# Kernel tuning notes

Hardware: AMD Instinct MI355X
Metric: run time of the kernel (lower is better)

The kernel has to match this reference:

```python
import jax, jax.numpy as jnp
import numpy as np

B, L, D = 4, 1024, 1024
H, DK, DV = 16, 64, 64
TEMP = float(np.power(DK, 0.5))
LN_EPS = 1e-5


def setup_inputs() -> dict:
    key = jax.random.key(0)
    ks = jax.random.split(key, 11)
    s_qk = np.sqrt(2.0 / (D + DK))
    s_v = np.sqrt(2.0 / (D + DV))
    inp = {
        'q_in': jax.random.normal(ks[0], (B, L, D), jnp.float32),
        'k_in': jax.random.normal(ks[1], (B, L, D), jnp.float32),
        'v_in': jax.random.normal(ks[2], (B, L, D), jnp.float32),
        'Wq':  jax.random.normal(ks[3], (D, H * DK), jnp.float32) * s_qk,
        'Wq2': jax.random.normal(ks[4], (D, H * DK), jnp.float32) * s_qk,
        'Wk':  jax.random.normal(ks[5], (D, H * DK), jnp.float32) * s_qk,
        'Wv':  jax.random.normal(ks[6], (D, H * DV), jnp.float32) * s_v,
        'Wo':  jax.random.normal(ks[7], (H * DV, D), jnp.float32) * np.sqrt(2.0 / (H * DV + D)),
        'ln_g': jnp.ones((D,), jnp.float32),
        'ln_b': jnp.zeros((D,), jnp.float32),
        'Er':  jax.random.normal(ks[8], (H, L, DK), jnp.float32),
        # causal mask: True above the diagonal (positions to be masked with -inf)
        'mask': jnp.triu(jnp.ones((L, L), jnp.bool_), k=1)[None].repeat(B, axis=0),
    }
    return inp


def _skew(rel):
    # rel: [H, B, Lq, Lr] with Lr == Lq. Music-Transformer skew:
    # pad one zero column on the left, reshape, drop first row.
    h, b, lq, lr = rel.shape
    rel = jnp.pad(rel, ((0, 0), (0, 0), (0, 0), (1, 0)))        # [H,B,Lq,Lr+1]
    rel = rel.reshape(h, b, lr + 1, lq)                          # [H,B,Lr+1,Lq]
    return rel[:, :, 1:, :].reshape(h, b, lq, lr)                # [H,B,Lq,Lr]


def reference(q_in, k_in, v_in, Wq, Wq2, Wk, Wv, Wo, ln_g, ln_b, Er, mask):
    residual = q_in
    # projections -> [H, B, L, d]
    def proj(x, W, d):
        return x.reshape(B * L, D).dot(W).reshape(B, L, H, d).transpose(2, 0, 1, 3)
    q = proj(q_in, Wq, DK)
    q2 = proj(q_in, Wq2, DK)
    k = proj(k_in, Wk, DK)
    v = proj(v_in, Wv, DV)

    attn = jnp.einsum('hbqd,hbkd->hbqk', q, k) / TEMP            # [H,B,Lq,Lk]
    rel = _skew(jnp.einsum('hbqd,hrd->hbqr', q2, Er)) / TEMP     # [H,B,Lq,Lk]

    m = mask[None]                                               # [1,B,Lq,Lk]
    neg = jnp.float32(-jnp.inf)
    attn = jnp.where(m, neg, attn)
    rel = jnp.where(m, neg, rel)
    p = jax.nn.softmax(attn + rel, axis=-1)                      # [H,B,Lq,Lk]

    out = jnp.einsum('hbqk,hbkd->hbqd', p, v)                    # [H,B,Lq,DV]
    out = out.transpose(1, 2, 0, 3).reshape(B, L, H * DV)
    out = out.dot(Wo)                                            # dropout is identity (eval)

    x = out + residual
    mu = x.mean(-1, keepdims=True)
    var = x.var(-1, keepdims=True)
    y = (x - mu) * jax.lax.rsqrt(var + LN_EPS) * ln_g + ln_b
    return y, p
```

## Files before the change

### kernel.cpp

```cpp
#include <hip/hip_runtime.h>

typedef __bf16 bf16;
typedef __bf16 v8bf __attribute__((ext_vector_type(8)));
typedef float v4f __attribute__((ext_vector_type(4)));
typedef unsigned int v4u __attribute__((ext_vector_type(4)));

#define B_ 4
#define L_ 1024
#define D_ 1024
#define NEG (-3.0e38f)
#define MFMA16(a, b, c) __builtin_amdgcn_mfma_f32_16x16x32_bf16(a, b, c, 0, 0, 0)

#define SWZ(base, r, cb) ((char*)(base) + ((r) * 128) + ((cb) ^ (((r) & 7) << 4)))

typedef const __attribute__((address_space(1))) void* gas_t;
typedef __attribute__((address_space(3))) void* las_t;
__device__ __forceinline__ void gl_lds16(const bf16* g, bf16* l)
{
    __builtin_amdgcn_global_load_lds((gas_t)g, (las_t)l, 16, 0, 0);
}

__global__ __launch_bounds__(256) void wconv_kernel(
    const float* __restrict__ w0, const float* __restrict__ w1,
    const float* __restrict__ w2, const float* __restrict__ w3,
    const float* __restrict__ w4, const float* __restrict__ er,
    const float* __restrict__ qin, const float* __restrict__ kin,
    const float* __restrict__ vin,
    bf16* __restrict__ wt, bf16* __restrict__ erb,
    bf16* __restrict__ qbf, bf16* __restrict__ kbf, bf16* __restrict__ vbf)
{
    int z = blockIdx.z;
    int tx = threadIdx.x, ty = threadIdx.y;
    if (z < 5) {
        const float* src = z == 0 ? w0 : z == 1 ? w1 : z == 2 ? w2 : z == 3 ? w3 : w4;
        bf16* dst = wt + (size_t)z * 1024 * 1024;
        __shared__ float t[32][33];
        int bx = blockIdx.x * 32, by = blockIdx.y * 32;
#pragma unroll
        for (int i = 0; i < 4; i++)
            t[ty + i * 8][tx] = src[(size_t)(by + ty + i * 8) * 1024 + bx + tx];
        __syncthreads();
#pragma unroll
        for (int i = 0; i < 4; i++)
            dst[(size_t)(bx + ty + i * 8) * 1024 + by + tx] = (bf16)t[tx][ty + i * 8];
    } else if (z == 5) {
        int base = (blockIdx.y * 32 + blockIdx.x) * 256 + ty * 32 + tx;
#pragma unroll
        for (int i = 0; i < 4; i++) {
            int idx = base + i * 262144;
            erb[idx] = (bf16)er[idx];
        }
    } else {
        const float* src = z == 6 ? qin : z == 7 ? kin : vin;
        bf16* dst = z == 6 ? qbf : z == 7 ? kbf : vbf;
        int id = (blockIdx.y * 32 + blockIdx.x) * 256 + ty * 32 + tx;
#pragma unroll
        for (int i = 0; i < 4; i++) {
            int j = id * 4 + i * 1048576;
            float4 v = *(const float4*)(src + j);
            union { bf16 h[4]; uint2 u; } t;
            t.h[0] = (bf16)v.x; t.h[1] = (bf16)v.y;
            t.h[2] = (bf16)v.z; t.h[3] = (bf16)v.w;
            *(uint2*)(dst + j) = t.u;
        }
    }
}

__global__ __launch_bounds__(256) void gemm64(
    const bf16* __restrict__ Ab, const bf16* __restrict__ Bt,
    float* __restrict__ Cf, bf16* __restrict__ Cb, bf16* __restrict__ Cb2,
    int K, int mode)
{
    __shared__ __align__(16) bf16 As[2][64 * 32];
    __shared__ __align__(16) bf16 Bs[2][128 * 32];
    int tid = threadIdx.x, lane = tid & 63, w = tid >> 6;
    int tn = blockIdx.x * 128, tm = blockIdx.y * 64;
    int wn = w * 32;
    int m15 = lane & 15, rq = lane >> 4, kq = rq * 8;

    v4f acc[4][2];
#pragma unroll
    for (int m = 0; m < 4; ++m)
#pragma unroll
        for (int n = 0; n < 2; ++n)
#pragma unroll
            for (int i = 0; i < 4; ++i) acc[m][n][i] = 0.f;

    int sr = lane >> 2, sc8 = (lane & 3) * 8;
    const bf16* ga  = Ab + (size_t)(tm + w * 16 + sr) * K + sc8;
    const bf16* gb0 = Bt + (size_t)(tn + w * 32 + sr) * K + sc8;
    const bf16* gb1 = gb0 + (size_t)16 * K;

#define GSTAGE(buf, k0s) { \
    gl_lds16(ga  + (k0s), As[buf] + w * 16 * 32); \
    gl_lds16(gb0 + (k0s), Bs[buf] + w * 32 * 32); \
    gl_lds16(gb1 + (k0s), Bs[buf] + (w * 32 + 16) * 32); }

    int cur = 0;
    GSTAGE(0, 0);
    __syncthreads();
    for (int k0 = 0; k0 < K; k0 += 32) {
        if (k0 + 32 < K) GSTAGE(cur ^ 1, k0 + 32);
        v8bf a[4], bb[2];
#pragma unroll
        for (int m = 0; m < 4; ++m)
            a[m] = *(const v8bf*)&As[cur][(m * 16 + m15) * 32 + kq];
#pragma unroll
        for (int n = 0; n < 2; ++n)
            bb[n] = *(const v8bf*)&Bs[cur][(wn + n * 16 + m15) * 32 + kq];
#pragma unroll
        for (int m = 0; m < 4; ++m)
#pragma unroll
            for (int n = 0; n < 2; ++n)
                acc[m][n] = MFMA16(a[m], bb[n], acc[m][n]);
        __syncthreads();
        cur ^= 1;
    }
#undef GSTAGE

#pragma unroll
    for (int m = 0; m < 4; ++m)
#pragma unroll
        for (int n = 0; n < 2; ++n) {
            int col = tn + wn + n * 16 + m15;
            if (mode == 2) {
                union { bf16 h[4]; uint2 u; } pk;
#pragma unroll
                for (int i = 0; i < 4; ++i) pk.h[i] = (bf16)acc[m][n][i];
                int row0 = tm + m * 16 + rq * 4;
                int bb2 = row0 >> 10, l = row0 & 1023, hh = col >> 6, dv = col & 63;
                *(uint2*)&Cb[(((size_t)(bb2 * 16 + hh) * 64 + dv) << 10) + l] = pk.u;
            } else {
#pragma unroll
                for (int i = 0; i < 4; ++i) {
                    int row = tm + m * 16 + rq * 4 + i;
                    float v = acc[m][n][i];
                    if (mode == 1) Cf[(size_t)row * 1024 + col] = v;
                    else {
                        bf16* dst = col < 1024 ? Cb : Cb2;
                        dst[(size_t)row * 1024 + (col & 1023)] = (bf16)v;
                    }
                }
            }
        }
}

__global__ __launch_bounds__(256, 2) void attn_mfma(
    const bf16* __restrict__ qb, const bf16* __restrict__ q2b,
    const bf16* __restrict__ kb, const bf16* __restrict__ vt,
    const bf16* __restrict__ erb, float* __restrict__ p_out,
    bf16* __restrict__ ab)
{
    int lin = blockIdx.x;
    int bh  = (lin & 7) | ((lin >> 6) << 3);
    int pp  = (lin >> 3) & 7;
    int h = bh >> 2, b = bh & 3;
    int tid = threadIdx.x, lane = tid & 63, w = tid >> 6;
    int m15 = lane & 15, rq = lane >> 4, kq = rq * 8;
    int li0 = w * 16 + rq * 4;

    __shared__ __align__(16) char KsB[2][8192];
    __shared__ __align__(16) char VtsB[2][8192];
    __shared__ __align__(16) char ErsB[3][8192];
    __shared__ __align__(16) float RELs[64][68];
    char* RELsB = (char*)RELs;

    size_t pb = (size_t)(h * 4 + b) << 20;
    size_t kbase = ((size_t)(b << 10) * 16 + h) * 64;
    size_t vbase = ((size_t)(b * 16 + h) << 16);
    const bf16* erh = erb + ((size_t)h << 16);

    int c0 = tid, c1 = tid + 256;
    int r0s = c0 >> 3, col0 = (c0 & 7) * 8, cb0 = (c0 & 7) * 16;
    int r1s = c1 >> 3, col1 = (c1 & 7) * 8, cb1 = (c1 & 7) * 16;

#define LOADK(d0, d1, kt) { int kk = (kt) << 6; \
    d0 = *(const uint4*)&kb[kbase + ((size_t)(kk + r0s) << 10) + col0]; \
    d1 = *(const uint4*)&kb[kbase + ((size_t)(kk + r1s) << 10) + col1]; }
#define LOADE(d0, d1, t) { const bf16* e = erh + ((size_t)(t) << 12); \
    d0 = *(const uint4*)&e[(r0s << 6) + col0]; \
    d1 = *(const uint4*)&e[(r1s << 6) + col1]; }
#define LOADV(d0, d1, kt) { int kk = (kt) << 6; \
    d0 = *(const uint4*)&vt[vbase + ((size_t)r0s << 10) + kk + col0]; \
    d1 = *(const uint4*)&vt[vbase + ((size_t)r1s << 10) + kk + col1]; }
#define STORE2(buf, v0, v1) { *(uint4*)SWZ(buf, r0s, cb0) = v0; \
                              *(uint4*)SWZ(buf, r1s, cb1) = v1; }

    for (int qs = 0; qs < 2; ++qs) {
        int qt = qs ? pp : 15 - pp;
        int q0 = qt << 6, nkt = qt + 1, t0 = 15 - qt;

        {
            int zr = tid >> 2, zc = (tid & 3) * 16;
            v4f zz = {0.f, 0.f, 0.f, 0.f};
            for (int kt = qt + 1; kt < 16; ++kt) {
                float* basep = p_out + pb + ((size_t)(q0 + zr) << 10) + kt * 64 + zc;
#pragma unroll
                for (int i = 0; i < 4; ++i)
                    __builtin_nontemporal_store(zz, (v4f*)(basep + i * 4));
            }
        }

        {
            uint4 a0 = *(const uint4*)&qb[((size_t)((b << 10) + q0 + r0s) * 16 + h) * 64 + col0];
            uint4 a1 = *(const uint4*)&qb[((size_t)((b << 10) + q0 + r1s) * 16 + h) * 64 + col1];
            uint4 b0 = *(const uint4*)&q2b[((size_t)((b << 10) + q0 + r0s) * 16 + h) * 64 + col0];
            uint4 b1 = *(const uint4*)&q2b[((size_t)((b << 10) + q0 + r1s) * 16 + h) * 64 + col1];
            STORE2(RELsB, a0, a1);
            STORE2(RELsB + 8192, b0, b1);
        }
        __syncthreads();
        v8bf alo  = *(const v8bf*)SWZ(RELsB,        w * 16 + m15, kq * 2);
        v8bf ahi  = *(const v8bf*)SWZ(RELsB,        w * 16 + m15, kq * 2 + 64);
        v8bf a2lo = *(const v8bf*)SWZ(RELsB + 8192, w * 16 + m15, kq * 2);
        v8bf a2hi = *(const v8bf*)SWZ(RELsB + 8192, w * 16 + m15, kq * 2 + 64);

        float m_run[4], l_run[4], linv[4];
#pragma unroll
        for (int i = 0; i < 4; ++i) { m_run[i] = NEG; l_run[i] = 0.f; }
        v4f oacc[4];
#pragma unroll
        for (int t = 0; t < 4; ++t)
#pragma unroll
            for (int i = 0; i < 4; ++i) oacc[t][i] = 0.f;

        for (int pass = 0; pass < 2; ++pass) {
            if (pass) {
#pragma unroll
                for (int i = 0; i < 4; ++i) linv[i] = 1.f / l_run[i];
            }
            {
                uint4 ka, kb2, e0a, e0b, e1a, e1b, va, vb2;
                LOADK(ka, kb2, 0);
                LOADE(e0a, e0b, t0);
                bool hb = (t0 + 1) <= 15;
                if (hb) LOADE(e1a, e1b, t0 + 1);
                if (pass) LOADV(va, vb2, 0);
                STORE2(KsB[0], ka, kb2);
                STORE2(ErsB[t0 % 3], e0a, e0b);
                if (hb) STORE2(ErsB[(t0 + 1) % 3], e1a, e1b);
                if (pass) STORE2(VtsB[0], va, vb2);
            }
            __syncthreads();

            uint4 nk0, nk1, ne0, ne1, nv0, nv1;
            for (int kt = 0; kt < nkt; ++kt) {
                int k0 = kt << 6;
                int tA = t0 + kt;
                bool hasB = tA < 15;
                bool hasNext = (kt + 1) < nkt;
                bool hasNE = hasNext && (tA + 2) <= 15;
                if (hasNext) {
                    LOADK(nk0, nk1, kt + 1);
                    if (hasNE) LOADE(ne0, ne1, tA + 2);
                    if (pass) LOADV(nv0, nv1, kt + 1);
                }
                char* Kb = KsB[kt & 1];
                char* EA = ErsB[tA % 3];
                char* EB = ErsB[(tA + 1) % 3];
                char* Vb = VtsB[kt & 1];

                __builtin_amdgcn_s_setprio(1);
#pragma unroll
                for (int ct = 0; ct < 4; ++ct) {
                    v4f a4 = {0.f, 0.f, 0.f, 0.f};
                    v8bf blo = *(const v8bf*)SWZ(EA, ct * 16 + m15, kq * 2);
                    v8bf bhi = *(const v8bf*)SWZ(EA, ct * 16 + m15, kq * 2 + 64);
                    a4 = MFMA16(a2lo, blo, a4);
                    a4 = MFMA16(a2hi, bhi, a4);
                    int c = ct * 16 + m15;
#pragma unroll
                    for (int i = 0; i < 4; ++i) {
                        int kl = c + li0 + i - 63;
                        if (kl >= 0) RELs[li0 + i][kl] = a4[i];
                    }
                }
                if (hasB) {
#pragma unroll
                    for (int ct = 0; ct < 4; ++ct) {
                        v4f a4 = {0.f, 0.f, 0.f, 0.f};
                        v8bf blo = *(const v8bf*)SWZ(EB, ct * 16 + m15, kq * 2);
                        v8bf bhi = *(const v8bf*)SWZ(EB, ct * 16 + m15, kq * 2 + 64);
                        a4 = MFMA16(a2lo, blo, a4);
                        a4 = MFMA16(a2hi, bhi, a4);
                        int c = ct * 16 + m15;
#pragma unroll
                        for (int i = 0; i < 4; ++i) {
                            int kl = c + li0 + i + 1;
                            if (kl < 64) RELs[li0 + i][kl] = a4[i];
                        }
                    }
                }
                v4f qk[4];
#pragma unroll
                for (int ct = 0; ct < 4; ++ct) {
                    v4f a4 = {0.f, 0.f, 0.f, 0.f};
                    v8bf blo = *(const v8bf*)SWZ(Kb, ct * 16 + m15, kq * 2);
                    v8bf bhi = *(const v8bf*)SWZ(Kb, ct * 16 + m15, kq * 2 + 64);
                    a4 = MFMA16(alo, blo, a4);
                    qk[ct] = MFMA16(ahi, bhi, a4);
                }
                __builtin_amdgcn_s_setprio(0);

                float sc[4][4];
#pragma unroll
                for (int ct = 0; ct < 4; ++ct)
#pragma unroll
                    for (int i = 0; i < 4; ++i) {
                        int li = li0 + i;
                        int j = ct * 16 + m15;
                        float v = (qk[ct][i] + RELs[li][j]) * 0.125f;
                        if (!hasB) v = (j > li) ? NEG : v;
                        sc[ct][i] = v;
                    }
                if (!pass) {
#pragma unroll
                    for (int i = 0; i < 4; ++i) {
                        float tmax = fmaxf(fmaxf(sc[0][i], sc[1][i]), fmaxf(sc[2][i], sc[3][i]));
#pragma unroll
                        for (int off = 1; off < 16; off <<= 1)
                            tmax = fmaxf(tmax, __shfl_xor(tmax, off));
                        float mn = fmaxf(m_run[i], tmax);
                        float es = __expf(sc[0][i] - mn) + __expf(sc[1][i] - mn)
                                 + __expf(sc[2][i] - mn) + __expf(sc[3][i] - mn);
#pragma unroll
                        for (int off = 1; off < 16; off <<= 1)
                            es += __shfl_xor(es, off);
                        l_run[i] = l_run[i] * __expf(m_run[i] - mn) + es;
                        m_run[i] = mn;
                    }
                } else {
#pragma unroll
                    for (int ct = 0; ct < 4; ++ct)
#pragma unroll
                        for (int i = 0; i < 4; ++i) {
                            int li = li0 + i;
                            int j = ct * 16 + m15;
                            RELs[li][j] = __expf(sc[ct][i] - m_run[i]) * linv[i];
                        }
                    asm volatile("" ::: "memory");
#pragma unroll
                    for (int i2 = 0; i2 < 2; ++i2)
#pragma unroll
                        for (int jh = 0; jh < 2; ++jh) {
                            int rr = w * 16 + (lane >> 3) + 8 * i2;
                            v4u val = *(const v4u*)(RELsB + rr * 272 + (lane & 7) * 16 + 128 * jh);
                            __builtin_nontemporal_store(val,
                                (v4u*)(p_out + pb + ((size_t)(q0 + rr) << 10) + k0 + (lane & 7) * 4 + 32 * jh));
                        }
                    const float* pr = &RELs[w * 16 + m15][0];
                    v4f f0 = *(const v4f*)(pr + kq);
                    v4f f1 = *(const v4f*)(pr + kq + 4);
                    v4f f2 = *(const v4f*)(pr + kq + 32);
                    v4f f3 = *(const v4f*)(pr + kq + 36);
                    v8bf plo, phi;
#pragma unroll
                    for (int j = 0; j < 4; ++j) {
                        plo[j] = (bf16)f0[j]; plo[j + 4] = (bf16)f1[j];
                        phi[j] = (bf16)f2[j]; phi[j + 4] = (bf16)f3[j];
                    }
                    __builtin_amdgcn_s_setprio(1);
#pragma unroll
                    for (int ct = 0; ct < 4; ++ct) {
                        v8bf blo = *(const v8bf*)SWZ(Vb, ct * 16 + m15, kq * 2);
                        v8bf bhi = *(const v8bf*)SWZ(Vb, ct * 16 + m15, kq * 2 + 64);
                        oacc[ct] = MFMA16(plo, blo, oacc[ct]);
                        oacc[ct] = MFMA16(phi, bhi, oacc[ct]);
                    }
                    __builtin_amdgcn_s_setprio(0);
                }
                if (hasNext) {
                    STORE2(KsB[(kt + 1) & 1], nk0, nk1);
                    if (hasNE) STORE2(ErsB[(tA + 2) % 3], ne0, ne1);
                    if (pass) STORE2(VtsB[(kt + 1) & 1], nv0, nv1);
                }
                __syncthreads();
            }
        }

#pragma unroll
        for (int ct = 0; ct < 4; ++ct)
#pragma unroll
            for (int i = 0; i < 4; ++i)
                ab[((size_t)((b << 10) + q0 + li0 + i) * 16 + h) * 64 + ct * 16 + m15] =
                    (bf16)oacc[ct][i];
    }
#undef LOADK
#undef LOADE
#undef LOADV
#undef STORE2
}

__global__ __launch_bounds__(256) void ln_kernel(
    const float* __restrict__ y0, const float* __restrict__ res,
    const float* __restrict__ g, const float* __restrict__ bb,
    float* __restrict__ y)
{
    int row = blockIdx.x, tid = threadIdx.x, lane = tid & 63, w = tid >> 6;
    __shared__ float rs[4], rq2[4];
    const float* xr = y0 + (size_t)row * D_;
    const float* rr = res + (size_t)row * D_;
    float x[4], sum = 0.f, sq = 0.f;
#pragma unroll
    for (int i = 0; i < 4; i++) {
        int c = tid + i * 256;
        x[i] = xr[c] + rr[c];
        sum += x[i]; sq += x[i] * x[i];
    }
#pragma unroll
    for (int off = 32; off; off >>= 1) { sum += __shfl_xor(sum, off); sq += __shfl_xor(sq, off); }
    if (lane == 0) { rs[w] = sum; rq2[w] = sq; }
    __syncthreads();
    sum = rs[0] + rs[1] + rs[2] + rs[3];
    sq  = rq2[0] + rq2[1] + rq2[2] + rq2[3];
    float mean = sum * (1.f / D_);
    float var  = sq * (1.f / D_) - mean * mean;
    float inv  = rsqrtf(var + 1e-5f);
#pragma unroll
    for (int i = 0; i < 4; i++) {
        int c = tid + i * 256;
        y[(size_t)row * D_ + c] = (x[i] - mean) * inv * g[c] + bb[c];
    }
}

extern "C" void kernel_launch(void* const* d_in, const int* in_sizes, int n_in,
                              void* d_out, int out_size, void* d_ws, size_t ws_size,
                              hipStream_t stream)
{
    const float* q_in = (const float*)d_in[0];
    const float* k_in = (const float*)d_in[1];
    const float* v_in = (const float*)d_in[2];
    const float* Wq   = (const float*)d_in[3];
    const float* Wq2  = (const float*)d_in[4];
    const float* Wk   = (const float*)d_in[5];
    const float* Wv   = (const float*)d_in[6];
    const float* Wo   = (const float*)d_in[7];
    const float* ln_g = (const float*)d_in[8];
    const float* ln_b = (const float*)d_in[9];
    const float* Er   = (const float*)d_in[10];

    float* y_out = (float*)d_out;
    float* p_out = y_out + (size_t)B_ * L_ * D_;

    char* ws = (char*)d_ws;
    const size_t MB = 1024 * 1024;
    bf16*  wT  = (bf16*)(ws);
    bf16*  erb = (bf16*)(ws + 10 * MB);
    bf16*  qb  = (bf16*)(ws + 12 * MB);
    bf16*  q2b = (bf16*)(ws + 20 * MB);
    bf16*  kb  = (bf16*)(ws + 28 * MB);
    bf16*  vtb = (bf16*)(ws + 36 * MB);
    bf16*  ab  = (bf16*)(ws + 44 * MB);
    float* y0  = (float*)(ws + 52 * MB);

    bf16* qbf = (bf16*)((char*)p_out + 160 * MB);
    bf16* kbf = (bf16*)((char*)p_out + 168 * MB);
    bf16* vbf = (bf16*)((char*)p_out + 176 * MB);

    wconv_kernel<<<dim3(32, 32, 9), dim3(32, 8), 0, stream>>>(
        Wq, Wq2, Wk, Wv, Wo, Er, q_in, k_in, v_in, wT, erb, qbf, kbf, vbf);

    gemm64<<<dim3(16, 64), 256, 0, stream>>>(qbf, wT,          nullptr, qb,  q2b,     1024, 0);
    gemm64<<<dim3( 8, 64), 256, 0, stream>>>(kbf, wT + 2 * MB, nullptr, kb,  nullptr, 1024, 0);
    gemm64<<<dim3( 8, 64), 256, 0, stream>>>(vbf, wT + 3 * MB, nullptr, vtb, nullptr, 1024, 2);

    attn_mfma<<<dim3(512), 256, 0, stream>>>(qb, q2b, kb, vtb, erb, p_out, ab);

    gemm64<<<dim3( 8, 64), 256, 0, stream>>>(ab, wT + 4 * MB, y0, nullptr, nullptr, 1024, 1);
    ln_kernel<<<4096, 256, 0, stream>>>(y0, q_in, ln_g, ln_b, y_out);
}
```

Before: 625.0 us.

## Drop LDS staging in attention kernel and read MFMA operands from global

The attention kernel no longer stages Q, Q2, K, V^T and Er tiles through swizzled LDS double and triple buffers. Each lane now loads its MFMA fragments straight from global memory, and the per-tile __syncthreads and register prefetch are removed. Launch bounds go from 2 to 4 blocks per CU to allow higher occupancy with the smaller LDS footprint. The aim is to cut LDS traffic and barrier stalls. The cost is that the four waves in a block each fetch the same K, V and Er data through the cache with strided, poorly coalesced 16-byte loads and no explicit prefetch.

```diff
diff --git a/kernel.cpp b/kernel.cpp
--- a/kernel.cpp
+++ b/kernel.cpp
@@ -10,8 +10,6 @@
 #define D_ 1024
 #define NEG (-3.0e38f)
 #define MFMA16(a, b, c) __builtin_amdgcn_mfma_f32_16x16x32_bf16(a, b, c, 0, 0, 0)
-
-#define SWZ(base, r, cb) ((char*)(base) + ((r) * 128) + ((cb) ^ (((r) & 7) << 4)))
 
 typedef const __attribute__((address_space(1))) void* gas_t;
 typedef __attribute__((address_space(3))) void* las_t;
@@ -145,7 +143,7 @@
         }
 }
 
-__global__ __launch_bounds__(256, 2) void attn_mfma(
+__global__ __launch_bounds__(256, 4) void attn_mfma(
     const bf16* __restrict__ qb, const bf16* __restrict__ q2b,
     const bf16* __restrict__ kb, const bf16* __restrict__ vt,
     const bf16* __restrict__ erb, float* __restrict__ p_out,
@@ -159,32 +157,12 @@
     int m15 = lane & 15, rq = lane >> 4, kq = rq * 8;
     int li0 = w * 16 + rq * 4;
 
-    __shared__ __align__(16) char KsB[2][8192];
-    __shared__ __align__(16) char VtsB[2][8192];
-    __shared__ __align__(16) char ErsB[3][8192];
-    __shared__ __align__(16) float RELs[64][68];
-    char* RELsB = (char*)RELs;
+    __shared__ float RELs[64][68];
 
     size_t pb = (size_t)(h * 4 + b) << 20;
     size_t kbase = ((size_t)(b << 10) * 16 + h) * 64;
     size_t vbase = ((size_t)(b * 16 + h) << 16);
     const bf16* erh = erb + ((size_t)h << 16);
-
-    int c0 = tid, c1 = tid + 256;
-    int r0s = c0 >> 3, col0 = (c0 & 7) * 8, cb0 = (c0 & 7) * 16;
-    int r1s = c1 >> 3, col1 = (c1 & 7) * 8, cb1 = (c1 & 7) * 16;
-
-#define LOADK(d0, d1, kt) { int kk = (kt) << 6; \
-    d0 = *(const uint4*)&kb[kbase + ((size_t)(kk + r0s) << 10) + col0]; \
-    d1 = *(const uint4*)&kb[kbase + ((size_t)(kk + r1s) << 10) + col1]; }
-#define LOADE(d0, d1, t) { const bf16* e = erh + ((size_t)(t) << 12); \
-    d0 = *(const uint4*)&e[(r0s << 6) + col0]; \
-    d1 = *(const uint4*)&e[(r1s << 6) + col1]; }
-#define LOADV(d0, d1, kt) { int kk = (kt) << 6; \
-    d0 = *(const uint4*)&vt[vbase + ((size_t)r0s << 10) + kk + col0]; \
-    d1 = *(const uint4*)&vt[vbase + ((size_t)r1s << 10) + kk + col1]; }
-#define STORE2(buf, v0, v1) { *(uint4*)SWZ(buf, r0s, cb0) = v0; \
-                              *(uint4*)SWZ(buf, r1s, cb1) = v1; }
 
     for (int qs = 0; qs < 2; ++qs) {
         int qt = qs ? pp : 15 - pp;
@@ -201,19 +179,12 @@
             }
         }
 
-        {
-            uint4 a0 = *(const uint4*)&qb[((size_t)((b << 10) + q0 + r0s) * 16 + h) * 64 + col0];
-            uint4 a1 = *(const uint4*)&qb[((size_t)((b << 10) + q0 + r1s) * 16 + h) * 64 + col1];
-            uint4 b0 = *(const uint4*)&q2b[((size_t)((b << 10) + q0 + r0s) * 16 + h) * 64 + col0];
-            uint4 b1 = *(const uint4*)&q2b[((size_t)((b << 10) + q0 + r1s) * 16 + h) * 64 + col1];
-            STORE2(RELsB, a0, a1);
-            STORE2(RELsB + 8192, b0, b1);
-        }
-        __syncthreads();
-        v8bf alo  = *(const v8bf*)SWZ(RELsB,        w * 16 + m15, kq * 2);
-        v8bf ahi  = *(const v8bf*)SWZ(RELsB,        w * 16 + m15, kq * 2 + 64);
-        v8bf a2lo = *(const v8bf*)SWZ(RELsB + 8192, w * 16 + m15, kq * 2);
-        v8bf a2hi = *(const v8bf*)SWZ(RELsB + 8192, w * 16 + m15, kq * 2 + 64);
+        const bf16* qrow  = &qb [((size_t)((b << 10) + q0 + w * 16 + m15) * 16 + h) * 64];
+        const bf16* q2row = &q2b[((size_t)((b << 10) + q0 + w * 16 + m15) * 16 + h) * 64];
+        v8bf alo  = *(const v8bf*)(qrow + kq);
+        v8bf ahi  = *(const v8bf*)(qrow + kq + 32);
+        v8bf a2lo = *(const v8bf*)(q2row + kq);
+        v8bf a2hi = *(const v8bf*)(q2row + kq + 32);
 
         float m_run[4], l_run[4], linv[4];
 #pragma unroll
@@ -229,45 +200,18 @@
 #pragma unroll
                 for (int i = 0; i < 4; ++i) linv[i] = 1.f / l_run[i];
             }
-            {
-                uint4 ka, kb2, e0a, e0b, e1a, e1b, va, vb2;
-                LOADK(ka, kb2, 0);
-                LOADE(e0a, e0b, t0);
-                bool hb = (t0 + 1) <= 15;
-                if (hb) LOADE(e1a, e1b, t0 + 1);
-                if (pass) LOADV(va, vb2, 0);
-                STORE2(KsB[0], ka, kb2);
-                STORE2(ErsB[t0 % 3], e0a, e0b);
-                if (hb) STORE2(ErsB[(t0 + 1) % 3], e1a, e1b);
-                if (pass) STORE2(VtsB[0], va, vb2);
-            }
-            __syncthreads();
-
-            uint4 nk0, nk1, ne0, ne1, nv0, nv1;
             for (int kt = 0; kt < nkt; ++kt) {
-                int k0 = kt << 6;
-                int tA = t0 + kt;
+                int k0 = kt << 6, tA = t0 + kt;
                 bool hasB = tA < 15;
-                bool hasNext = (kt + 1) < nkt;
-                bool hasNE = hasNext && (tA + 2) <= 15;
-                if (hasNext) {
-                    LOADK(nk0, nk1, kt + 1);
-                    if (hasNE) LOADE(ne0, ne1, tA + 2);
-                    if (pass) LOADV(nv0, nv1, kt + 1);
-                }
-                char* Kb = KsB[kt & 1];
-                char* EA = ErsB[tA % 3];
-                char* EB = ErsB[(tA + 1) % 3];
-                char* Vb = VtsB[kt & 1];
+                const bf16* eA = erh + ((size_t)tA << 12);
 
                 __builtin_amdgcn_s_setprio(1);
 #pragma unroll
                 for (int ct = 0; ct < 4; ++ct) {
+                    const bf16* er_ = eA + (ct * 16 + m15) * 64;
                     v4f a4 = {0.f, 0.f, 0.f, 0.f};
-                    v8bf blo = *(const v8bf*)SWZ(EA, ct * 16 + m15, kq * 2);
-                    v8bf bhi = *(const v8bf*)SWZ(EA, ct * 16 + m15, kq * 2 + 64);
-                    a4 = MFMA16(a2lo, blo, a4);
-                    a4 = MFMA16(a2hi, bhi, a4);
+                    a4 = MFMA16(a2lo, *(const v8bf*)(er_ + kq), a4);
+                    a4 = MFMA16(a2hi, *(const v8bf*)(er_ + kq + 32), a4);
                     int c = ct * 16 + m15;
 #pragma unroll
                     for (int i = 0; i < 4; ++i) {
@@ -276,13 +220,13 @@
                     }
                 }
                 if (hasB) {
+                    const bf16* eB = eA + 4096;
 #pragma unroll
                     for (int ct = 0; ct < 4; ++ct) {
+                        const bf16* er_ = eB + (ct * 16 + m15) * 64;
                         v4f a4 = {0.f, 0.f, 0.f, 0.f};
-                        v8bf blo = *(const v8bf*)SWZ(EB, ct * 16 + m15, kq * 2);
-                        v8bf bhi = *(const v8bf*)SWZ(EB, ct * 16 + m15, kq * 2 + 64);
-                        a4 = MFMA16(a2lo, blo, a4);
-                        a4 = MFMA16(a2hi, bhi, a4);
+                        a4 = MFMA16(a2lo, *(const v8bf*)(er_ + kq), a4);
+                        a4 = MFMA16(a2hi, *(const v8bf*)(er_ + kq + 32), a4);
                         int c = ct * 16 + m15;
 #pragma unroll
                         for (int i = 0; i < 4; ++i) {
@@ -294,11 +238,10 @@
                 v4f qk[4];
 #pragma unroll
                 for (int ct = 0; ct < 4; ++ct) {
+                    const bf16* kr = kb + kbase + (size_t)(k0 + ct * 16 + m15) * 1024;
                     v4f a4 = {0.f, 0.f, 0.f, 0.f};
-                    v8bf blo = *(const v8bf*)SWZ(Kb, ct * 16 + m15, kq * 2);
-                    v8bf bhi = *(const v8bf*)SWZ(Kb, ct * 16 + m15, kq * 2 + 64);
-                    a4 = MFMA16(alo, blo, a4);
-                    qk[ct] = MFMA16(ahi, bhi, a4);
+                    a4 = MFMA16(alo, *(const v8bf*)(kr + kq), a4);
+                    qk[ct] = MFMA16(ahi, *(const v8bf*)(kr + kq + 32), a4);
                 }
                 __builtin_amdgcn_s_setprio(0);
 
@@ -344,9 +287,11 @@
 #pragma unroll
                         for (int jh = 0; jh < 2; ++jh) {
                             int rr = w * 16 + (lane >> 3) + 8 * i2;
-                            v4u val = *(const v4u*)(RELsB + rr * 272 + (lane & 7) * 16 + 128 * jh);
+                            v4u val = *(const v4u*)((const char*)&RELs[rr][0]
+                                                    + (lane & 7) * 16 + 128 * jh);
                             __builtin_nontemporal_store(val,
-                                (v4u*)(p_out + pb + ((size_t)(q0 + rr) << 10) + k0 + (lane & 7) * 4 + 32 * jh));
+                                (v4u*)(p_out + pb + ((size_t)(q0 + rr) << 10) + k0
+                                       + (lane & 7) * 4 + 32 * jh));
                         }
                     const float* pr = &RELs[w * 16 + m15][0];
                     v4f f0 = *(const v4f*)(pr + kq);
@@ -362,19 +307,12 @@
                     __builtin_amdgcn_s_setprio(1);
 #pragma unroll
                     for (int ct = 0; ct < 4; ++ct) {
-                        v8bf blo = *(const v8bf*)SWZ(Vb, ct * 16 + m15, kq * 2);
-                        v8bf bhi = *(const v8bf*)SWZ(Vb, ct * 16 + m15, kq * 2 + 64);
-                        oacc[ct] = MFMA16(plo, blo, oacc[ct]);
-                        oacc[ct] = MFMA16(phi, bhi, oacc[ct]);
+                        const bf16* vr = vt + vbase + (size_t)(ct * 16 + m15) * 1024 + k0;
+                        oacc[ct] = MFMA16(plo, *(const v8bf*)(vr + kq), oacc[ct]);
+                        oacc[ct] = MFMA16(phi, *(const v8bf*)(vr + kq + 32), oacc[ct]);
                     }
                     __builtin_amdgcn_s_setprio(0);
                 }
-                if (hasNext) {
-                    STORE2(KsB[(kt + 1) & 1], nk0, nk1);
-                    if (hasNE) STORE2(ErsB[(tA + 2) % 3], ne0, ne1);
-                    if (pass) STORE2(VtsB[(kt + 1) & 1], nv0, nv1);
-                }
-                __syncthreads();
             }
         }
 
@@ -385,10 +323,6 @@
                 ab[((size_t)((b << 10) + q0 + li0 + i) * 16 + h) * 64 + ct * 16 + m15] =
                     (bf16)oacc[ct][i];
     }
-#undef LOADK
-#undef LOADE
-#undef LOADV
-#undef STORE2
 }
 
 __global__ __launch_bounds__(256) void ln_kernel(
@@ -464,7 +398,7 @@
     gemm64<<<dim3( 8, 64), 256, 0, stream>>>(kbf, wT + 2 * MB, nullptr, kb,  nullptr, 1024, 0);
     gemm64<<<dim3( 8, 64), 256, 0, stream>>>(vbf, wT + 3 * MB, nullptr, vtb, nullptr, 1024, 2);
 
-    attn_mfma<<<dim3(512), 256, 0, stream>>>(qb, q2b, kb, vtb, erb, p_out, ab);
+    attn_mfma<<<dim3(512), dim3(256), 0, stream>>>(qb, q2b, kb, vtb, erb, p_out, ab);
 
     gemm64<<<dim3( 8, 64), 256, 0, stream>>>(ab, wT + 4 * MB, y0, nullptr, nullptr, 1024, 1);
     ln_kernel<<<4096, 256, 0, stream>>>(y0, q_in, ln_g, ln_b, y_out);
```

Result: slower. 668.9 us (+7.0%).

## Use 128x128 GEMM tiles and merge Q/K/V projections into one launch

Applied to the files above, without the earlier changes.

Replaces the 64x128 GEMM tile with a 128x128 tile using a 2x2 wave layout, so each wave computes 64x64 and reuses more operand data per LDS load. The three projection GEMMs are fused into a single launch that dispatches on blockIdx.x, removing two launches and filling the GPU with more blocks at once. The double-buffered LDS prefetch is dropped in favour of a single buffer with load-sync-compute-sync, which may expose global load latency. The output GEMM uses the same larger tile but gets only 256 blocks.

```diff
diff --git a/kernel.cpp b/kernel.cpp
--- a/kernel.cpp
+++ b/kernel.cpp
@@ -66,74 +66,69 @@
     }
 }
 
-__global__ __launch_bounds__(256) void gemm64(
+__device__ __forceinline__ void gemm128_core(
     const bf16* __restrict__ Ab, const bf16* __restrict__ Bt,
     float* __restrict__ Cf, bf16* __restrict__ Cb, bf16* __restrict__ Cb2,
-    int K, int mode)
-{
-    __shared__ __align__(16) bf16 As[2][64 * 32];
-    __shared__ __align__(16) bf16 Bs[2][128 * 32];
+    int K, int mode, int tn, int tm,
+    bf16* __restrict__ As , bf16* __restrict__ Bs )
+{
     int tid = threadIdx.x, lane = tid & 63, w = tid >> 6;
-    int tn = blockIdx.x * 128, tm = blockIdx.y * 64;
-    int wn = w * 32;
+    int wm = (w & 1) * 64, wn = (w >> 1) * 64;
     int m15 = lane & 15, rq = lane >> 4, kq = rq * 8;
 
-    v4f acc[4][2];
+    v4f acc[4][4];
 #pragma unroll
     for (int m = 0; m < 4; ++m)
 #pragma unroll
-        for (int n = 0; n < 2; ++n)
+        for (int n = 0; n < 4; ++n)
 #pragma unroll
             for (int i = 0; i < 4; ++i) acc[m][n][i] = 0.f;
 
-    int sr = lane >> 2, sc8 = (lane & 3) * 8;
-    const bf16* ga  = Ab + (size_t)(tm + w * 16 + sr) * K + sc8;
-    const bf16* gb0 = Bt + (size_t)(tn + w * 32 + sr) * K + sc8;
-    const bf16* gb1 = gb0 + (size_t)16 * K;
-
-#define GSTAGE(buf, k0s) { \
-    gl_lds16(ga  + (k0s), As[buf] + w * 16 * 32); \
-    gl_lds16(gb0 + (k0s), Bs[buf] + w * 32 * 32); \
-    gl_lds16(gb1 + (k0s), Bs[buf] + (w * 32 + 16) * 32); }
-
-    int cur = 0;
-    GSTAGE(0, 0);
-    __syncthreads();
+    int sr = lane >> 2, scb = (lane & 3) * 8;
+    const bf16* ga = Ab + (size_t)(tm + w * 32 + sr) * K + scb;
+    const bf16* gb = Bt + (size_t)(tn + w * 32 + sr) * K + scb;
+    bf16* la = As + w * 32 * 32;
+    bf16* lb = Bs + w * 32 * 32;
+    const size_t rowskip = (size_t)16 * K;
+
     for (int k0 = 0; k0 < K; k0 += 32) {
-        if (k0 + 32 < K) GSTAGE(cur ^ 1, k0 + 32);
-        v8bf a[4], bb[2];
+        gl_lds16(ga + k0, la);
+        gl_lds16(ga + k0 + rowskip, la + 512);
+        gl_lds16(gb + k0, lb);
+        gl_lds16(gb + k0 + rowskip, lb + 512);
+        __syncthreads();
+
+        v8bf a[4], bfr[4];
 #pragma unroll
         for (int m = 0; m < 4; ++m)
-            a[m] = *(const v8bf*)&As[cur][(m * 16 + m15) * 32 + kq];
-#pragma unroll
-        for (int n = 0; n < 2; ++n)
-            bb[n] = *(const v8bf*)&Bs[cur][(wn + n * 16 + m15) * 32 + kq];
+            a[m] = *(const v8bf*)&As[(wm + m * 16 + m15) * 32 + kq];
+#pragma unroll
+        for (int n = 0; n < 4; ++n)
+            bfr[n] = *(const v8bf*)&Bs[(wn + n * 16 + m15) * 32 + kq];
 #pragma unroll
         for (int m = 0; m < 4; ++m)
 #pragma unroll
-            for (int n = 0; n < 2; ++n)
-                acc[m][n] = MFMA16(a[m], bb[n], acc[m][n]);
+            for (int n = 0; n < 4; ++n)
+                acc[m][n] = MFMA16(a[m], bfr[n], acc[m][n]);
         __syncthreads();
-        cur ^= 1;
     }
-#undef GSTAGE
 
 #pragma unroll
     for (int m = 0; m < 4; ++m)
 #pragma unroll
-        for (int n = 0; n < 2; ++n) {
+        for (int n = 0; n < 4; ++n) {
             int col = tn + wn + n * 16 + m15;
             if (mode == 2) {
                 union { bf16 h[4]; uint2 u; } pk;
 #pragma unroll
                 for (int i = 0; i < 4; ++i) pk.h[i] = (bf16)acc[m][n][i];
-                int row0 = tm + m * 16 + rq * 4;
+                int row0 = tm + wm + m * 16 + rq * 4;
                 int bb2 = row0 >> 10, l = row0 & 1023, hh = col >> 6, dv = col & 63;
                 *(uint2*)&Cb[(((size_t)(bb2 * 16 + hh) * 64 + dv) << 10) + l] = pk.u;
             } else {
 #pragma unroll
                 for (int i = 0; i < 4; ++i) {
-                    int row = tm + m * 16 + rq * 4 + i;
+                    int row = tm + wm + m * 16 + rq * 4 + i;
                     float v = acc[m][n][i];
                     if (mode == 1) Cf[(size_t)row * 1024 + col] = v;
                     else {
@@ -143,6 +138,36 @@
                 }
             }
         }
+}
+
+__global__ __launch_bounds__(256) void gemm_proj(
+    const bf16* __restrict__ qbf, const bf16* __restrict__ kbf,
+    const bf16* __restrict__ vbf, const bf16* __restrict__ wT,
+    bf16* __restrict__ qb, bf16* __restrict__ q2b,
+    bf16* __restrict__ kb, bf16* __restrict__ vtb)
+{
+    __shared__ __align__(16) bf16 As[128 * 32];
+    __shared__ __align__(16) bf16 Bs[128 * 32];
+    int bx = blockIdx.x, tm = blockIdx.y * 128;
+    const size_t MB = 1024 * 1024;
+    if (bx < 16)
+        gemm128_core(qbf, wT, nullptr, qb, q2b, 1024, 0, bx * 128, tm, As, Bs);
+    else if (bx < 24)
+        gemm128_core(kbf, wT + 2 * MB, nullptr, kb, nullptr, 1024, 0,
+                     (bx - 16) * 128, tm, As, Bs);
+    else
+        gemm128_core(vbf, wT + 3 * MB, nullptr, vtb, nullptr, 1024, 2,
+                     (bx - 24) * 128, tm, As, Bs);
+}
+
+__global__ __launch_bounds__(256) void gemm_out(
+    const bf16* __restrict__ ab, const bf16* __restrict__ woT,
+    float* __restrict__ y0)
+{
+    __shared__ __align__(16) bf16 As[128 * 32];
+    __shared__ __align__(16) bf16 Bs[128 * 32];
+    gemm128_core(ab, woT, y0, nullptr, nullptr, 1024, 1,
+                 blockIdx.x * 128, blockIdx.y * 128, As, Bs);
 }
 
 __global__ __launch_bounds__(256, 2) void attn_mfma(
@@ -460,12 +485,11 @@
     wconv_kernel<<<dim3(32, 32, 9), dim3(32, 8), 0, stream>>>(
         Wq, Wq2, Wk, Wv, Wo, Er, q_in, k_in, v_in, wT, erb, qbf, kbf, vbf);
 
-    gemm64<<<dim3(16, 64), 256, 0, stream>>>(qbf, wT,          nullptr, qb,  q2b,     1024, 0);
-    gemm64<<<dim3( 8, 64), 256, 0, stream>>>(kbf, wT + 2 * MB, nullptr, kb,  nullptr, 1024, 0);
-    gemm64<<<dim3( 8, 64), 256, 0, stream>>>(vbf, wT + 3 * MB, nullptr, vtb, nullptr, 1024, 2);
-
-    attn_mfma<<<dim3(512), 256, 0, stream>>>(qb, q2b, kb, vtb, erb, p_out, ab);
-
-    gemm64<<<dim3( 8, 64), 256, 0, stream>>>(ab, wT + 4 * MB, y0, nullptr, nullptr, 1024, 1);
+    gemm_proj<<<dim3(32, 32), 256, 0, stream>>>(qbf, kbf, vbf, wT,
+                                                qb, q2b, kb, vtb);
+
+    attn_mfma<<<dim3(512), dim3(256), 0, stream>>>(qb, q2b, kb, vtb, erb, p_out, ab);
+
+    gemm_out<<<dim3(8, 32), 256, 0, stream>>>(ab, wT + 4 * MB, y0);
     ln_kernel<<<4096, 256, 0, stream>>>(y0, q_in, ln_g, ln_b, y_out);
 }
```

After: 606.7 us. 1.03x faster.
